# Optimization experiments

Hardware: AMD Instinct MI355X
Metric: run time of the kernel (lower is better)

The kernel has to match this reference:

```python
import jax, jax.numpy as jnp
import numpy as np

B, C, H, W = 8, 64, 128, 128
G, DGPG = 4, 1
GD = G * DGPG          # total deformable groups = 4
COUT = 64
KH = KW = 3
K = KH * KW            # 9 kernel locations
PAD = STR = DIL = 1
HO, WO = 128, 128      # same padding, stride 1
OFFSET_SCALE = 1.0
CDG = C // GD          # channels per deformable group = 16
CPG = C // G           # input channels per conv group = 16
KOFF = 7
POFF = 3


def dwconv7(x, w, b):
    # depthwise 7x7 conv, groups == channels; w: [C,1,7,7]
    y = jax.lax.conv_general_dilated(
        x, w, window_strides=(1, 1), padding=[(POFF, POFF), (POFF, POFF)],
        feature_group_count=C, dimension_numbers=('NCHW', 'OIHW', 'NCHW'))
    return y + b[None, :, None, None]


def gn1(x, g, b):
    # GroupNorm with a single group: normalize over (C,H,W) per sample
    m = x.mean(axis=(1, 2, 3), keepdims=True)
    v = x.var(axis=(1, 2, 3), keepdims=True)
    return (x - m) * jax.lax.rsqrt(v + 1e-5) * g[None, :, None, None] + b[None, :, None, None]


def pw(x, w, b):
    # 1x1 conv; w: [O, C]
    return jnp.einsum('bchw,oc->bohw', x, w) + b[None, :, None, None]


def setup_inputs() -> dict:
    key = jax.random.key(0)
    ks = jax.random.split(key, 8)
    s = 0.02
    return {
        'x': jax.random.normal(ks[0], (B, C, H, W), jnp.float32),
        'w_dw_off': jax.random.normal(ks[1], (C, 1, KOFF, KOFF), jnp.float32) * s,
        'b_dw_off': jnp.zeros((C,), jnp.float32),
        'gn_off_g': jnp.ones((C,), jnp.float32),
        'gn_off_b': jnp.zeros((C,), jnp.float32),
        'w_pw_off': jax.random.normal(ks[2], (GD * K * 2, C), jnp.float32) * s,
        'b_pw_off': jnp.zeros((GD * K * 2,), jnp.float32),
        'w_dw_m': jax.random.normal(ks[3], (C, 1, KOFF, KOFF), jnp.float32) * s,
        'b_dw_m': jnp.zeros((C,), jnp.float32),
        'gn_m_g': jnp.ones((C,), jnp.float32),
        'gn_m_b': jnp.zeros((C,), jnp.float32),
        'w_pw_m': jax.random.normal(ks[4], (GD * K, C), jnp.float32) * s,
        'b_pw_m': jnp.zeros((GD * K,), jnp.float32),
        'weight': jax.random.normal(ks[5], (COUT, CPG, KH, KW), jnp.float32) * s,
        'bias': jax.random.normal(ks[6], (COUT,), jnp.float32) * s,
    }


def _deform_conv(x, offset, mask, weight, bias):
    # offset: [B, GD, K, 2, HO, WO] (y, x); mask: [B, GD, K, HO, WO] (softmaxed)
    ky, kx = jnp.meshgrid(jnp.arange(KH), jnp.arange(KW), indexing='ij')
    ky = ky.reshape(K).astype(x.dtype)
    kx = kx.reshape(K).astype(x.dtype)
    oy = jnp.arange(HO, dtype=x.dtype)
    ox = jnp.arange(WO, dtype=x.dtype)
    base_y = oy[None, :] * STR - PAD + ky[:, None] * DIL   # [K, HO]
    base_x = ox[None, :] * STR - PAD + kx[:, None] * DIL   # [K, WO]
    py = base_y[None, None, :, :, None] + offset[:, :, :, 0] * OFFSET_SCALE  # [B,GD,K,HO,WO]
    px = base_x[None, None, :, None, :] + offset[:, :, :, 1] * OFFSET_SCALE

    x_flat = x.reshape(B, GD, CDG, H * W)
    y0 = jnp.floor(py)
    x0 = jnp.floor(px)
    wy = py - y0
    wx = px - x0

    def gather(yi, xi):
        valid = ((yi >= 0) & (yi < H) & (xi >= 0) & (xi < W)).astype(x.dtype)
        yc = jnp.clip(yi, 0, H - 1).astype(jnp.int32)
        xc = jnp.clip(xi, 0, W - 1).astype(jnp.int32)
        idx = (yc * W + xc).reshape(B, GD, 1, K * HO * WO)
        v = jnp.take_along_axis(x_flat, idx, axis=3).reshape(B, GD, CDG, K, HO, WO)
        return v * valid[:, :, None]

    v = (gather(y0, x0) * ((1 - wy) * (1 - wx))[:, :, None]
         + gather(y0, x0 + 1) * ((1 - wy) * wx)[:, :, None]
         + gather(y0 + 1, x0) * (wy * (1 - wx))[:, :, None]
         + gather(y0 + 1, x0 + 1) * (wy * wx)[:, :, None])
    v = v * mask[:, :, None]                               # modulated samples
    v = v.reshape(B, G, CPG, K, HO, WO)
    wg = weight.reshape(G, COUT // G, CPG, K)
    out = jnp.einsum('bgckhw,gock->bgohw', v, wg).reshape(B, COUT, HO, WO)
    return out + bias[None, :, None, None]


def reference(x, w_dw_off, b_dw_off, gn_off_g, gn_off_b, w_pw_off, b_pw_off,
              w_dw_m, b_dw_m, gn_m_g, gn_m_b, w_pw_m, b_pw_m, weight, bias):
    off = pw(gn1(dwconv7(x, w_dw_off, b_dw_off), gn_off_g, gn_off_b), w_pw_off, b_pw_off)
    m = pw(gn1(dwconv7(x, w_dw_m, b_dw_m), gn_m_g, gn_m_b), w_pw_m, b_pw_m)
    offset = off.reshape(B, GD, K, 2, HO, WO)
    mask = jax.nn.softmax(m.reshape(B, GD, K, HO, WO), axis=2)  # attn over kernel points
    return _deform_conv(x, offset, mask, weight, bias)
```

## Files before the change

kernel.cpp:

```cpp
#include <hip/hip_runtime.h>
#include <hip/hip_fp16.h>
#include <math.h>

#define HW     16384
#define IMG_H  128
#define IMG_W  128

typedef _Float16 f16x2 __attribute__((ext_vector_type(2)));
typedef __fp16 fp16v2 __attribute__((ext_vector_type(2)));
typedef _Float16 f16x4 __attribute__((ext_vector_type(4)));
typedef float f32x4 __attribute__((ext_vector_type(4)));

#define OFF_T2    ((size_t)0)
#define OFF_XT    ((size_t)8388608)
#define OFF_WT    ((size_t)12582912)
#define OFF_PART  ((size_t)12599040)
#define OFF_WB    ((size_t)19711744)
#define OFF_WDW2  ((size_t)19716352)
#define OFF_WBO   ((size_t)19719936)
#define OFF_WBM   ((size_t)19752704)
#define OFF_DC    ((size_t)19769088)

__global__ void k_prep(const float* __restrict__ wpw_off,
                       const float* __restrict__ wpw_m,
                       const float* __restrict__ wdef,
                       const float* __restrict__ wdwo,
                       const float* __restrict__ wdwm,
                       float* __restrict__ ws) {
    int i = blockIdx.x * 256 + threadIdx.x;
    if (i < 6912) {
        int c = i / 108, o = i % 108;
        ws[OFF_WT + i] = (o < 72) ? wpw_off[o * 64 + c] : wpw_m[(o - 72) * 64 + c];
    } else if (i < 9216) {
        int j = i - 6912;
        int lane = j & 63;
        int gt = j >> 6;
        int tap = gt % 9, g = gt / 9;
        int oc = lane & 15, qh = lane >> 4;
        union { ushort h[4]; uint2 u; } pk;
#pragma unroll
        for (int jj = 0; jj < 4; ++jj) {
            float wv = wdef[((g * 16 + oc) * 16 + (4 * qh + jj)) * 9 + tap];
            pk.h[jj] = __half_as_ushort(__float2half(wv));
        }
        ((uint2*)(ws + OFF_WB))[j] = pk.u;
    } else if (i < 12800) {
        int j = i - 9216;
        int q = j & 3;
        int r = j >> 2;
        int dy = r % 7;
        int cv = (r / 7) & 1;
        int c = r / 14;
        const float* src = cv ? wdwm : wdwo;
        int dx0 = q * 2;
        float w0 = src[c * 49 + dy * 7 + dx0];
        float w1 = (dx0 + 1 < 7) ? src[c * 49 + dy * 7 + dx0 + 1] : 0.f;
        union { __half h[2]; uint u; } pk;
        pk.h[0] = __float2half(w0);
        pk.h[1] = __float2half(w1);
        ((uint*)(ws + OFF_WDW2))[j] = pk.u;
    }
}

__global__ __launch_bounds__(256) void k_trans(const float* __restrict__ x,
                                               __half* __restrict__ xT) {
    int n = blockIdx.x * 256 + threadIdx.x;
    int p = n & (HW - 1);
    int bg = n >> 14;
    const float* src = x + (size_t)bg * 16 * HW + p;
    union { __half2 h2[8]; uint4 u[2]; } pk;
#pragma unroll
    for (int i = 0; i < 8; ++i) {
        float a = src[(size_t)(2 * i) * HW];
        float bq = src[(size_t)(2 * i + 1) * HW];
        pk.h2[i] = __halves2half2(__float2half(a), __float2half(bq));
    }
    uint4* dst = (uint4*)(xT + (size_t)n * 16);
    dst[0] = pk.u[0];
    dst[1] = pk.u[1];
}

__global__ __launch_bounds__(256) void k_dw(const float* __restrict__ x,
                                            const float* __restrict__ bdwo,
                                            const float* __restrict__ bdwm,
                                            const uint* __restrict__ wdw2,
                                            uint2* __restrict__ t2p,
                                            float* __restrict__ partial) {
    int bid = blockIdx.x;
    int b = bid >> 9;
    int c2 = (bid >> 4) & 31;
    int stripe = (bid & 15) * 8;
    int t = threadIdx.x;
    int cb = t & 31;
    int row = stripe + (t >> 5);
    int c0 = c2 * 2;

    float vo[2][4], vm[2][4];
    float s1o = 0.f, s2o = 0.f, s1m = 0.f, s2m = 0.f;
    union CV { fp16v2 v; f16x2 h; };
    union WU { uint u; f16x2 h; };

#pragma unroll
    for (int ch = 0; ch < 2; ++ch) {
        int c = c0 + ch;
        const float4* pl = (const float4*)(x + ((size_t)(b * 64 + c)) * HW);
        const uint* wp = wdw2 + c * 56;
        float acco[4] = {0.f, 0.f, 0.f, 0.f};
        float accm[4] = {0.f, 0.f, 0.f, 0.f};
#pragma unroll
        for (int dy = 0; dy < 7; ++dy) {
            int iy = row - 3 + dy;
            if (iy >= 0 && iy < IMG_H) {
                const float4* prow = pl + iy * 32;
                float4 f4 = prow[cb];
                float4 f4m = prow[cb == 0 ? 0 : cb - 1];
                float4 f4p = prow[cb == 31 ? 31 : cb + 1];
                bool le = (cb == 0), re = (cb == 31);
                float v[11];
                v[0] = le ? 0.f : f4m.y;
                v[1] = le ? 0.f : f4m.z;
                v[2] = le ? 0.f : f4m.w;
                v[3] = f4.x; v[4] = f4.y; v[5] = f4.z; v[6] = f4.w;
                v[7] = re ? 0.f : f4p.x;
                v[8] = re ? 0.f : f4p.y;
                v[9] = re ? 0.f : f4p.z;
                v[10] = re ? 0.f : f4p.w;
                f16x2 hp[10];
#pragma unroll
                for (int d = 0; d < 10; ++d) {
                    CV cv;
                    cv.v = __builtin_amdgcn_cvt_pkrtz(v[d], v[d + 1]);
                    hp[d] = cv.h;
                }
#pragma unroll
                for (int cc = 0; cc < 4; ++cc) {
                    WU w0, w1, w2, w3, u0, u1, u2, u3;
                    w0.u = wp[dy * 4 + 0]; w1.u = wp[dy * 4 + 1];
                    w2.u = wp[dy * 4 + 2]; w3.u = wp[dy * 4 + 3];
                    u0.u = wp[28 + dy * 4 + 0]; u1.u = wp[28 + dy * 4 + 1];
                    u2.u = wp[28 + dy * 4 + 2]; u3.u = wp[28 + dy * 4 + 3];
                    float ao = acco[cc], am = accm[cc];
                    ao = __builtin_amdgcn_fdot2(hp[cc],     w0.h, ao, false);
                    ao = __builtin_amdgcn_fdot2(hp[cc + 2], w1.h, ao, false);
                    ao = __builtin_amdgcn_fdot2(hp[cc + 4], w2.h, ao, false);
                    ao = __builtin_amdgcn_fdot2(hp[cc + 6], w3.h, ao, false);
                    am = __builtin_amdgcn_fdot2(hp[cc],     u0.h, am, false);
                    am = __builtin_amdgcn_fdot2(hp[cc + 2], u1.h, am, false);
                    am = __builtin_amdgcn_fdot2(hp[cc + 4], u2.h, am, false);
                    am = __builtin_amdgcn_fdot2(hp[cc + 6], u3.h, am, false);
                    acco[cc] = ao; accm[cc] = am;
                }
            }
        }
        float bo = bdwo[c], bm = bdwm[c];
#pragma unroll
        for (int cc = 0; cc < 4; ++cc) {
            float o_ = acco[cc] + bo, m_ = accm[cc] + bm;
            vo[ch][cc] = o_; vm[ch][cc] = m_;
            s1o += o_; s2o += o_ * o_; s1m += m_; s2m += m_ * m_;
        }
    }

    union { uint2 u2[4]; uint4 u4[2]; } ot;
#pragma unroll
    for (int cc = 0; cc < 4; ++cc) {
        ot.u2[cc].x = (uint)__half_as_ushort(__float2half(vo[0][cc])) |
                      ((uint)__half_as_ushort(__float2half(vo[1][cc])) << 16);
        ot.u2[cc].y = (uint)__half_as_ushort(__float2half(vm[0][cc])) |
                      ((uint)__half_as_ushort(__float2half(vm[1][cc])) << 16);
    }
    uint4* dst = (uint4*)(t2p + ((size_t)(b * 32 + c2) * HW + row * IMG_W + cb * 4));
    dst[0] = ot.u4[0];
    dst[1] = ot.u4[1];

#pragma unroll
    for (int d = 32; d; d >>= 1) {
        s1o += __shfl_down(s1o, d);
        s2o += __shfl_down(s2o, d);
        s1m += __shfl_down(s1m, d);
        s2m += __shfl_down(s2m, d);
    }
    __shared__ float red[4][4];
    if ((t & 63) == 0) {
        int w = t >> 6;
        red[w][0] = s1o; red[w][1] = s2o; red[w][2] = s1m; red[w][3] = s2m;
    }
    __syncthreads();
    if (t < 4) {
        float v = red[0][t] + red[1][t] + red[2][t] + red[3][t];
        partial[(size_t)bid * 4 + t] = v;
    }
}

__global__ __launch_bounds__(256) void k_finfold(const float* __restrict__ partial,
                      const float* __restrict__ gog, const float* __restrict__ gob,
                      const float* __restrict__ gmg, const float* __restrict__ gmb,
                      const float* __restrict__ wT,
                      const float* __restrict__ bpo,
                      const float* __restrict__ bpm,
                      uint2* __restrict__ wbo,
                      uint2* __restrict__ wbm,
                      float* __restrict__ dconst) {
    __shared__ float adsh[256];
    int b = blockIdx.x, t = threadIdx.x;
    {
        const float4* pp = (const float4*)partial + (size_t)b * 512;
        float4 s = make_float4(0.f, 0.f, 0.f, 0.f);
#pragma unroll
        for (int i = 0; i < 2; ++i) {
            float4 v = pp[t + i * 256];
            s.x += v.x; s.y += v.y; s.z += v.z; s.w += v.w;
        }
#pragma unroll
        for (int d = 32; d; d >>= 1) {
            s.x += __shfl_down(s.x, d);
            s.y += __shfl_down(s.y, d);
            s.z += __shfl_down(s.z, d);
            s.w += __shfl_down(s.w, d);
        }
        __shared__ float red[4][4];
        if ((t & 63) == 0) {
            int w = t >> 6;
            red[w][0] = s.x; red[w][1] = s.y; red[w][2] = s.z; red[w][3] = s.w;
        }
        __syncthreads();
        if (t < 64) {
            float s1o = red[0][0] + red[1][0] + red[2][0] + red[3][0];
            float s2o = red[0][1] + red[1][1] + red[2][1] + red[3][1];
            float s1m = red[0][2] + red[1][2] + red[2][2] + red[3][2];
            float s2m = red[0][3] + red[1][3] + red[2][3] + red[3][3];
            int c = t;
            const float invN = 1.f / 1048576.f;
            float m_o = s1o * invN;
            float v_o = s2o * invN - m_o * m_o;
            float i_o = rsqrtf(v_o + 1e-5f);
            float m_m = s1m * invN;
            float v_m = s2m * invN - m_m * m_m;
            float i_m = rsqrtf(v_m + 1e-5f);
            adsh[c * 4 + 0] = i_o * gog[c];
            adsh[c * 4 + 1] = gob[c] - m_o * (i_o * gog[c]);
            adsh[c * 4 + 2] = i_m * gmg[c];
            adsh[c * 4 + 3] = gmb[c] - m_m * (i_m * gmg[c]);
        }
        __syncthreads();
    }
    for (int i = t; i < 2048; i += 256) {
        int lane = i & 63;
        int f = i >> 6;
        int g = f >> 3, kk = (f >> 1) & 3, nf = f & 1;
        int n = lane & 15, q = lane >> 4;
        int out = nf * 16 + n;
        union { ushort h[4]; uint2 u; } pk;
#pragma unroll
        for (int jj = 0; jj < 4; ++jj) {
            int ch = kk * 16 + 4 * q + jj;
            float w = (out < 18) ? adsh[ch * 4 + 0] * wT[ch * 108 + g * 18 + out] : 0.f;
            pk.h[jj] = __half_as_ushort(__float2half(w));
        }
        wbo[((size_t)(b * 4) + g) * 8 * 64 + (size_t)(kk * 2 + nf) * 64 + lane] = pk.u;
    }
    for (int i = t; i < 1024; i += 256) {
        int lane = i & 63;
        int f = i >> 6;
        int g = f >> 2, kk = f & 3;
        int n = lane & 15, q = lane >> 4;
        union { ushort h[4]; uint2 u; } pk;
#pragma unroll
        for (int jj = 0; jj < 4; ++jj) {
            int ch = kk * 16 + 4 * q + jj;
            float w = (n < 9) ? adsh[ch * 4 + 2] * wT[ch * 108 + 72 + g * 9 + n] : 0.f;
            pk.h[jj] = __half_as_ushort(__float2half(w));
        }
        wbm[((size_t)(b * 4) + g) * 4 * 64 + (size_t)kk * 64 + lane] = pk.u;
    }
    if (t < 108) {
        float s = (t < 72) ? bpo[t] : bpm[t - 72];
        for (int c = 0; c < 64; ++c) {
            float d = (t < 72) ? adsh[c * 4 + 1] : adsh[c * 4 + 3];
            s = fmaf(d, wT[c * 108 + t], s);
        }
        dconst[b * 108 + t] = s;
    }
}

__global__ __launch_bounds__(256, 4) void k_gthf(const uint2* __restrict__ t2p,
                                                 const uint2* __restrict__ wbo,
                                                 const uint2* __restrict__ wbm,
                                                 const float* __restrict__ dconst,
                                                 const __half* __restrict__ xT,
                                                 const uint2* __restrict__ wb,
                                                 const float* __restrict__ bias,
                                                 float* __restrict__ out) {
    __shared__ union SMem {
        struct {
            uint4 xsA[506];
            uint4 xsB[506];
            uint  slab[5120];
        } s;
        float shout[4864];
    } sm;

    int tid = threadIdx.x;
    int bid = blockIdx.x;
    int bg = bid >> 6;
    int tile = bid & 63;
    int tr = tile >> 3, tc = tile & 7;
    int r0 = tr * 16, c0 = tc * 16;
    int g = bg & 3, b = bg >> 2;
    int wr0 = r0 - 3, wc0 = c0 - 3;

    const __half* xg = xT + (size_t)bg * HW * 16;

    int sidx[2];
    uint4 sA[2], sB[2];
#pragma unroll
    for (int it = 0; it < 2; ++it) {
        int idx = tid + it * 256;
        sidx[it] = -1;
        if (idx < 484) {
            int ly = idx / 22, lx = idx - ly * 22;
            int sr = wr0 + ly; sr = sr < 0 ? 0 : (sr > 127 ? 127 : sr);
            int sc = wc0 + lx; sc = sc < 0 ? 0 : (sc > 127 ? 127 : sc);
            const uint4* src = (const uint4*)(xg + (size_t)(sr * IMG_W + sc) * 16);
            sA[it] = src[0];
            sB[it] = src[1];
            sidx[it] = ly * 23 + lx;
        }
    }

    int row = r0 + (tid >> 4), col = c0 + (tid & 15);
    int p = row * IMG_W + col;
    int lane = tid & 63, wv = tid >> 6;
    int m_idx = lane & 15, q_idx = lane >> 4;

    union BU { uint2 u; f16x4 h; };

    const uint2* wboP = wbo + ((size_t)(b * 4) + g) * 8 * 64 + lane;
    const uint2* wbmP = wbm + ((size_t)(b * 4) + g) * 4 * 64 + lane;
    f16x4 bO[8], bM[4];
#pragma unroll
    for (int i = 0; i < 8; ++i) { BU t; t.u = wboP[i * 64]; bO[i] = t.h; }
#pragma unroll
    for (int i = 0; i < 4; ++i) { BU t; t.u = wbmP[i * 64]; bM[i] = t.h; }

    uint* aslab = sm.s.slab + wv * 1280;
    const uint2* tp = t2p + (size_t)b * 32 * HW + p;

    f32x4 accO0[4], accO1[4], accM[4];
#pragma unroll
    for (int s = 0; s < 4; ++s) {
        accO0[s] = (f32x4){0.f, 0.f, 0.f, 0.f};
        accO1[s] = (f32x4){0.f, 0.f, 0.f, 0.f};
        accM[s]  = (f32x4){0.f, 0.f, 0.f, 0.f};
    }

    uint2 cur[8], nxt[8];
#pragma unroll
    for (int j = 0; j < 8; ++j) cur[j] = tp[(size_t)j * HW];

#pragma unroll
    for (int kk = 0; kk < 4; ++kk) {
        if (kk < 3) {
#pragma unroll
            for (int j = 0; j < 8; ++j) nxt[j] = tp[(size_t)((kk + 1) * 8 + j) * HW];
        }
        uint* rowp = aslab + lane * 20;
        ((uint4*)rowp)[0] = make_uint4(cur[0].x, cur[1].x, cur[2].x, cur[3].x);
        ((uint4*)rowp)[1] = make_uint4(cur[4].x, cur[5].x, cur[6].x, cur[7].x);
        ((uint4*)(rowp + 8))[0] = make_uint4(cur[0].y, cur[1].y, cur[2].y, cur[3].y);
        ((uint4*)(rowp + 8))[1] = make_uint4(cur[4].y, cur[5].y, cur[6].y, cur[7].y);
#pragma unroll
        for (int s = 0; s < 4; ++s) {
            const uint* pr = aslab + (s * 16 + m_idx) * 20 + 2 * q_idx;
            BU ao, am;
            ao.u = *(const uint2*)pr;
            am.u = *(const uint2*)(pr + 8);
            accO0[s] = __builtin_amdgcn_mfma_f32_16x16x16f16(ao.h, bO[kk * 2 + 0], accO0[s], 0, 0, 0);
            accO1[s] = __builtin_amdgcn_mfma_f32_16x16x16f16(ao.h, bO[kk * 2 + 1], accO1[s], 0, 0, 0);
            accM[s]  = __builtin_amdgcn_mfma_f32_16x16x16f16(am.h, bM[kk], accM[s], 0, 0, 0);
        }
#pragma unroll
        for (int j = 0; j < 8; ++j) cur[j] = nxt[j];
    }

#pragma unroll
    for (int it = 0; it < 2; ++it)
        if (sidx[it] >= 0) {
            sm.s.xsA[sidx[it]] = sA[it];
            sm.s.xsB[sidx[it]] = sB[it];
        }

    const float* dc = dconst + b * 108;

#pragma unroll
    for (int s = 0; s < 4; ++s)
#pragma unroll
        for (int j = 0; j < 4; ++j) {
            int px = s * 16 + 4 * q_idx + j;
            union { __half2 h2; uint u; } pk;
            pk.h2 = __halves2half2(__float2half(accO0[s][j]),
                                   __float2half(accO1[s][j]));
            aslab[px * 20 + m_idx] = pk.u;
        }
    float facc[18];
    {
        const uint4* dr = (const uint4*)(aslab + lane * 20);
        uint4 d0 = dr[0], d1 = dr[1], d2 = dr[2], d3 = dr[3];
        uint du[16] = {d0.x, d0.y, d0.z, d0.w, d1.x, d1.y, d1.z, d1.w,
                       d2.x, d2.y, d2.z, d2.w, d3.x, d3.y, d3.z, d3.w};
        union { uint u; __half2 h2; } cv;
#pragma unroll
        for (int i = 0; i < 16; ++i) {
            cv.u = du[i];
            float2 f = __half22float2(cv.h2);
            facc[i] = f.x + dc[g * 18 + i];
            if (i < 2) facc[16 + i] = f.y + dc[g * 18 + 16 + i];
        }
    }

    float macc[9];
    {
        float* fsl = (float*)aslab;
#pragma unroll
        for (int s = 0; s < 4; ++s)
#pragma unroll
            for (int j = 0; j < 4; ++j) {
                int px = s * 16 + 4 * q_idx + j;
                fsl[px * 20 + m_idx] = accM[s][j];
            }
#pragma unroll
        for (int k = 0; k < 9; ++k) macc[k] = fsl[lane * 20 + k] + dc[72 + g * 9 + k];
        float mx = macc[0];
#pragma unroll
        for (int k = 1; k < 9; ++k) mx = fmaxf(mx, macc[k]);
        float ssum = 0.f;
#pragma unroll
        for (int k = 0; k < 9; ++k) {
            float e = __expf(macc[k] - mx);
            macc[k] = e;
            ssum += e;
        }
        float inv = 1.f / ssum;
#pragma unroll
        for (int k = 0; k < 9; ++k) macc[k] *= inv;
    }

    const uint2* wbp = wb + (size_t)(g * 9) * 64 + lane;
    f16x4 bfr[9];
#pragma unroll
    for (int k = 0; k < 9; ++k) { BU t; t.u = wbp[k * 64]; bfr[k] = t.h; }

    __syncthreads();

    uint4* shvw = (uint4*)aslab + lane * 3;
    const _Float16* shvh = (const _Float16*)aslab;

    f32x4 acc[4];
#pragma unroll
    for (int s = 0; s < 4; ++s) acc[s] = (f32x4){0.f, 0.f, 0.f, 0.f};

#pragma unroll
    for (int k = 0; k < 9; ++k) {
        float mk = macc[k];
        float py = (float)(row + k / 3 - 1) + facc[k * 2 + 0];
        float px = (float)(col + k % 3 - 1) + facc[k * 2 + 1];
        float y0f = floorf(py), x0f = floorf(px);
        float wy = py - y0f, wx = px - x0f;
        int iy0 = (int)y0f, ix0 = (int)x0f;
        int iy1 = iy0 + 1, ix1 = ix0 + 1;
        float fy0 = (iy0 >= 0 && iy0 < IMG_H) ? (1.f - wy) : 0.f;
        float fy1 = (iy1 >= 0 && iy1 < IMG_H) ? wy : 0.f;
        float fx0 = (ix0 >= 0 && ix0 < IMG_W) ? (1.f - wx) : 0.f;
        float fx1 = (ix1 >= 0 && ix1 < IMG_W) ? wx : 0.f;
        __half2 f00h = __float2half2_rn(fy0 * fx0 * mk);
        __half2 f01h = __float2half2_rn(fy0 * fx1 * mk);
        __half2 f10h = __float2half2_rn(fy1 * fx0 * mk);
        __half2 f11h = __float2half2_rn(fy1 * fx1 * mk);
        int ly0 = iy0 - wr0; ly0 = ly0 < 0 ? 0 : (ly0 > 21 ? 21 : ly0);
        int ly1 = iy1 - wr0; ly1 = ly1 < 0 ? 0 : (ly1 > 21 ? 21 : ly1);
        int lx0 = ix0 - wc0; lx0 = lx0 < 0 ? 0 : (lx0 > 21 ? 21 : lx0);
        int lx1 = ix1 - wc0; lx1 = lx1 < 0 ? 0 : (lx1 > 21 ? 21 : lx1);
        int i00 = ly0 * 23 + lx0, i01 = ly0 * 23 + lx1;
        int i10 = ly1 * 23 + lx0, i11 = ly1 * 23 + lx1;
        union Q8 { uint4 u[2]; __half2 h2[8]; };
        Q8 q00, q01, q10, q11;
        q00.u[0] = sm.s.xsA[i00]; q00.u[1] = sm.s.xsB[i00];
        q01.u[0] = sm.s.xsA[i01]; q01.u[1] = sm.s.xsB[i01];
        q10.u[0] = sm.s.xsA[i10]; q10.u[1] = sm.s.xsB[i10];
        q11.u[0] = sm.s.xsA[i11]; q11.u[1] = sm.s.xsB[i11];
        union V8 { __half2 h2[4]; uint4 u; };
        V8 pa, pb;
#pragma unroll
        for (int i = 0; i < 4; ++i) {
            __half2 vh = __hmul2(f00h, q00.h2[i]);
            vh = __hfma2(f01h, q01.h2[i], vh);
            vh = __hfma2(f10h, q10.h2[i], vh);
            vh = __hfma2(f11h, q11.h2[i], vh);
            pa.h2[i] = vh;
        }
#pragma unroll
        for (int i = 4; i < 8; ++i) {
            __half2 vh = __hmul2(f00h, q00.h2[i]);
            vh = __hfma2(f01h, q01.h2[i], vh);
            vh = __hfma2(f10h, q10.h2[i], vh);
            vh = __hfma2(f11h, q11.h2[i], vh);
            pb.h2[i - 4] = vh;
        }
        shvw[0] = pa.u;
        shvw[1] = pb.u;
#pragma unroll
        for (int s = 0; s < 4; ++s) {
            f16x4 af = *(const f16x4*)(shvh +
                        ((size_t)(s * 16 + m_idx)) * 24 + q_idx * 4);
            acc[s] = __builtin_amdgcn_mfma_f32_16x16x16f16(af, bfr[k], acc[s], 0, 0, 0);
        }
    }

    __syncthreads();

#pragma unroll
    for (int s = 0; s < 4; ++s)
#pragma unroll
        for (int j = 0; j < 4; ++j)
            sm.shout[(wv * 64 + s * 16 + 4 * q_idx + j) * 19 + m_idx] = acc[s][j];

    float* outp = out + ((size_t)b * 64 + g * 16) * HW + p;
#pragma unroll
    for (int o = 0; o < 16; ++o)
        outp[(size_t)o * HW] = sm.shout[tid * 19 + o] + bias[g * 16 + o];
}

extern "C" void kernel_launch(void* const* d_in, const int* in_sizes, int n_in,
                              void* d_out, int out_size, void* d_ws, size_t ws_size,
                              hipStream_t stream) {
    const float* x        = (const float*)d_in[0];
    const float* w_dw_off = (const float*)d_in[1];
    const float* b_dw_off = (const float*)d_in[2];
    const float* gn_off_g = (const float*)d_in[3];
    const float* gn_off_b = (const float*)d_in[4];
    const float* w_pw_off = (const float*)d_in[5];
    const float* b_pw_off = (const float*)d_in[6];
    const float* w_dw_m   = (const float*)d_in[7];
    const float* b_dw_m   = (const float*)d_in[8];
    const float* gn_m_g   = (const float*)d_in[9];
    const float* gn_m_b   = (const float*)d_in[10];
    const float* w_pw_m   = (const float*)d_in[11];
    const float* b_pw_m   = (const float*)d_in[12];
    const float* weight   = (const float*)d_in[13];
    const float* bias     = (const float*)d_in[14];

    float* ws = (float*)d_ws;
    uint2* t2p    = (uint2*)(ws + OFF_T2);
    __half* xT    = (__half*)(ws + OFF_XT);
    float* wT     = ws + OFF_WT;
    float* part   = ws + OFF_PART;
    const uint2* wb = (const uint2*)(ws + OFF_WB);
    const uint* wdw2 = (const uint*)(ws + OFF_WDW2);
    uint2* wbo    = (uint2*)(ws + OFF_WBO);
    uint2* wbm    = (uint2*)(ws + OFF_WBM);
    float* dconst = ws + OFF_DC;

    k_prep<<<50, 256, 0, stream>>>(w_pw_off, w_pw_m, weight, w_dw_off, w_dw_m, ws);
    k_trans<<<2048, 256, 0, stream>>>(x, xT);
    k_dw<<<4096, 256, 0, stream>>>(x, b_dw_off, b_dw_m, wdw2, t2p, part);
    k_finfold<<<8, 256, 0, stream>>>(part, gn_off_g, gn_off_b, gn_m_g, gn_m_b,
                                     wT, b_pw_off, b_pw_m, wbo, wbm, dconst);
    k_gthf<<<2048, 256, 0, stream>>>(t2p, wbo, wbm, dconst, xT, wb, bias, (float*)d_out);
}
```

Baseline: 103.7 us.

## Fuse x transpose into depthwise kernel and restructure gather kernel loads

```diff
diff --git a/kernel.cpp b/kernel.cpp
--- a/kernel.cpp
+++ b/kernel.cpp
@@ -62,29 +62,12 @@
     }
 }
 
-__global__ __launch_bounds__(256) void k_trans(const float* __restrict__ x,
-                                               __half* __restrict__ xT) {
-    int n = blockIdx.x * 256 + threadIdx.x;
-    int p = n & (HW - 1);
-    int bg = n >> 14;
-    const float* src = x + (size_t)bg * 16 * HW + p;
-    union { __half2 h2[8]; uint4 u[2]; } pk;
-#pragma unroll
-    for (int i = 0; i < 8; ++i) {
-        float a = src[(size_t)(2 * i) * HW];
-        float bq = src[(size_t)(2 * i + 1) * HW];
-        pk.h2[i] = __halves2half2(__float2half(a), __float2half(bq));
-    }
-    uint4* dst = (uint4*)(xT + (size_t)n * 16);
-    dst[0] = pk.u[0];
-    dst[1] = pk.u[1];
-}
-
 __global__ __launch_bounds__(256) void k_dw(const float* __restrict__ x,
                                             const float* __restrict__ bdwo,
                                             const float* __restrict__ bdwm,
                                             const uint* __restrict__ wdw2,
                                             uint2* __restrict__ t2p,
+                                            __half* __restrict__ xT,
                                             float* __restrict__ partial) {
     int bid = blockIdx.x;
     int b = bid >> 9;
@@ -96,6 +79,7 @@
     int c0 = c2 * 2;
 
     float vo[2][4], vm[2][4];
+    float4 cen[2];
     float s1o = 0.f, s2o = 0.f, s1m = 0.f, s2m = 0.f;
     union CV { fp16v2 v; f16x2 h; };
     union WU { uint u; f16x2 h; };
@@ -115,6 +99,7 @@
                 float4 f4 = prow[cb];
                 float4 f4m = prow[cb == 0 ? 0 : cb - 1];
                 float4 f4p = prow[cb == 31 ? 31 : cb + 1];
+                if (dy == 3) cen[ch] = f4;
                 bool le = (cb == 0), re = (cb == 31);
                 float v[11];
                 v[0] = le ? 0.f : f4m.y;
@@ -173,6 +158,19 @@
     dst[0] = ot.u4[0];
     dst[1] = ot.u4[1];
 
+    {
+        int bg = b * 4 + (c0 >> 4);
+        int cw = c0 & 15;
+        uint* xtw = (uint*)(xT + ((size_t)bg * HW + row * IMG_W + cb * 4) * 16 + cw);
+        float ca[4] = {cen[0].x, cen[0].y, cen[0].z, cen[0].w};
+        float cbv[4] = {cen[1].x, cen[1].y, cen[1].z, cen[1].w};
+#pragma unroll
+        for (int j = 0; j < 4; ++j) {
+            xtw[j * 8] = (uint)__half_as_ushort(__float2half(ca[j])) |
+                         ((uint)__half_as_ushort(__float2half(cbv[j])) << 16);
+        }
+    }
+
 #pragma unroll
     for (int d = 32; d; d >>= 1) {
         s1o += __shfl_down(s1o, d);
@@ -311,20 +309,16 @@
 
     const __half* xg = xT + (size_t)bg * HW * 16;
 
-    int sidx[2];
-    uint4 sA[2], sB[2];
 #pragma unroll
     for (int it = 0; it < 2; ++it) {
         int idx = tid + it * 256;
-        sidx[it] = -1;
         if (idx < 484) {
             int ly = idx / 22, lx = idx - ly * 22;
             int sr = wr0 + ly; sr = sr < 0 ? 0 : (sr > 127 ? 127 : sr);
             int sc = wc0 + lx; sc = sc < 0 ? 0 : (sc > 127 ? 127 : sc);
             const uint4* src = (const uint4*)(xg + (size_t)(sr * IMG_W + sc) * 16);
-            sA[it] = src[0];
-            sB[it] = src[1];
-            sidx[it] = ly * 23 + lx;
+            sm.s.xsA[ly * 23 + lx] = src[0];
+            sm.s.xsB[ly * 23 + lx] = src[1];
         }
     }
 
@@ -343,6 +337,11 @@
 #pragma unroll
     for (int i = 0; i < 4; ++i) { BU t; t.u = wbmP[i * 64]; bM[i] = t.h; }
 
+    const uint2* wbp = wb + (size_t)(g * 9) * 64 + lane;
+    f16x4 bfr[9];
+#pragma unroll
+    for (int k = 0; k < 9; ++k) { BU t; t.u = wbp[k * 64]; bfr[k] = t.h; }
+
     uint* aslab = sm.s.slab + wv * 1280;
     const uint2* tp = t2p + (size_t)b * 32 * HW + p;
 
@@ -354,21 +353,16 @@
         accM[s]  = (f32x4){0.f, 0.f, 0.f, 0.f};
     }
 
-    uint2 cur[8], nxt[8];
-#pragma unroll
-    for (int j = 0; j < 8; ++j) cur[j] = tp[(size_t)j * HW];
-
 #pragma unroll
     for (int kk = 0; kk < 4; ++kk) {
-        if (kk < 3) {
-#pragma unroll
-            for (int j = 0; j < 8; ++j) nxt[j] = tp[(size_t)((kk + 1) * 8 + j) * HW];
-        }
+        uint2 v[8];
+#pragma unroll
+        for (int j = 0; j < 8; ++j) v[j] = tp[(size_t)(kk * 8 + j) * HW];
         uint* rowp = aslab + lane * 20;
-        ((uint4*)rowp)[0] = make_uint4(cur[0].x, cur[1].x, cur[2].x, cur[3].x);
-        ((uint4*)rowp)[1] = make_uint4(cur[4].x, cur[5].x, cur[6].x, cur[7].x);
-        ((uint4*)(rowp + 8))[0] = make_uint4(cur[0].y, cur[1].y, cur[2].y, cur[3].y);
-        ((uint4*)(rowp + 8))[1] = make_uint4(cur[4].y, cur[5].y, cur[6].y, cur[7].y);
+        ((uint4*)rowp)[0] = make_uint4(v[0].x, v[1].x, v[2].x, v[3].x);
+        ((uint4*)rowp)[1] = make_uint4(v[4].x, v[5].x, v[6].x, v[7].x);
+        ((uint4*)(rowp + 8))[0] = make_uint4(v[0].y, v[1].y, v[2].y, v[3].y);
+        ((uint4*)(rowp + 8))[1] = make_uint4(v[4].y, v[5].y, v[6].y, v[7].y);
 #pragma unroll
         for (int s = 0; s < 4; ++s) {
             const uint* pr = aslab + (s * 16 + m_idx) * 20 + 2 * q_idx;
@@ -379,16 +373,7 @@
             accO1[s] = __builtin_amdgcn_mfma_f32_16x16x16f16(ao.h, bO[kk * 2 + 1], accO1[s], 0, 0, 0);
             accM[s]  = __builtin_amdgcn_mfma_f32_16x16x16f16(am.h, bM[kk], accM[s], 0, 0, 0);
         }
-#pragma unroll
-        for (int j = 0; j < 8; ++j) cur[j] = nxt[j];
-    }
-
-#pragma unroll
-    for (int it = 0; it < 2; ++it)
-        if (sidx[it] >= 0) {
-            sm.s.xsA[sidx[it]] = sA[it];
-            sm.s.xsB[sidx[it]] = sB[it];
-        }
+    }
 
     const float* dc = dconst + b * 108;
 
@@ -418,7 +403,6 @@
         }
     }
 
-    float macc[9];
     {
         float* fsl = (float*)aslab;
 #pragma unroll
@@ -428,6 +412,7 @@
                 int px = s * 16 + 4 * q_idx + j;
                 fsl[px * 20 + m_idx] = accM[s][j];
             }
+        float macc[9];
 #pragma unroll
         for (int k = 0; k < 9; ++k) macc[k] = fsl[lane * 20 + k] + dc[72 + g * 9 + k];
         float mx = macc[0];
@@ -443,91 +428,86 @@
         float inv = 1.f / ssum;
 #pragma unroll
         for (int k = 0; k < 9; ++k) macc[k] *= inv;
-    }
-
-    const uint2* wbp = wb + (size_t)(g * 9) * 64 + lane;
-    f16x4 bfr[9];
-#pragma unroll
-    for (int k = 0; k < 9; ++k) { BU t; t.u = wbp[k * 64]; bfr[k] = t.h; }
-
-    __syncthreads();
-
-    uint4* shvw = (uint4*)aslab + lane * 3;
-    const _Float16* shvh = (const _Float16*)aslab;
-
-    f32x4 acc[4];
-#pragma unroll
-    for (int s = 0; s < 4; ++s) acc[s] = (f32x4){0.f, 0.f, 0.f, 0.f};
-
-#pragma unroll
-    for (int k = 0; k < 9; ++k) {
-        float mk = macc[k];
-        float py = (float)(row + k / 3 - 1) + facc[k * 2 + 0];
-        float px = (float)(col + k % 3 - 1) + facc[k * 2 + 1];
-        float y0f = floorf(py), x0f = floorf(px);
-        float wy = py - y0f, wx = px - x0f;
-        int iy0 = (int)y0f, ix0 = (int)x0f;
-        int iy1 = iy0 + 1, ix1 = ix0 + 1;
-        float fy0 = (iy0 >= 0 && iy0 < IMG_H) ? (1.f - wy) : 0.f;
-        float fy1 = (iy1 >= 0 && iy1 < IMG_H) ? wy : 0.f;
-        float fx0 = (ix0 >= 0 && ix0 < IMG_W) ? (1.f - wx) : 0.f;
-        float fx1 = (ix1 >= 0 && ix1 < IMG_W) ? wx : 0.f;
-        __half2 f00h = __float2half2_rn(fy0 * fx0 * mk);
-        __half2 f01h = __float2half2_rn(fy0 * fx1 * mk);
-        __half2 f10h = __float2half2_rn(fy1 * fx0 * mk);
-        __half2 f11h = __float2half2_rn(fy1 * fx1 * mk);
-        int ly0 = iy0 - wr0; ly0 = ly0 < 0 ? 0 : (ly0 > 21 ? 21 : ly0);
-        int ly1 = iy1 - wr0; ly1 = ly1 < 0 ? 0 : (ly1 > 21 ? 21 : ly1);
-        int lx0 = ix0 - wc0; lx0 = lx0 < 0 ? 0 : (lx0 > 21 ? 21 : lx0);
-        int lx1 = ix1 - wc0; lx1 = lx1 < 0 ? 0 : (lx1 > 21 ? 21 : lx1);
-        int i00 = ly0 * 23 + lx0, i01 = ly0 * 23 + lx1;
-        int i10 = ly1 * 23 + lx0, i11 = ly1 * 23 + lx1;
-        union Q8 { uint4 u[2]; __half2 h2[8]; };
-        Q8 q00, q01, q10, q11;
-        q00.u[0] = sm.s.xsA[i00]; q00.u[1] = sm.s.xsB[i00];
-        q01.u[0] = sm.s.xsA[i01]; q01.u[1] = sm.s.xsB[i01];
-        q10.u[0] = sm.s.xsA[i10]; q10.u[1] = sm.s.xsB[i10];
-        q11.u[0] = sm.s.xsA[i11]; q11.u[1] = sm.s.xsB[i11];
-        union V8 { __half2 h2[4]; uint4 u; };
-        V8 pa, pb;
-#pragma unroll
-        for (int i = 0; i < 4; ++i) {
-            __half2 vh = __hmul2(f00h, q00.h2[i]);
-            vh = __hfma2(f01h, q01.h2[i], vh);
-            vh = __hfma2(f10h, q10.h2[i], vh);
-            vh = __hfma2(f11h, q11.h2[i], vh);
-            pa.h2[i] = vh;
-        }
-#pragma unroll
-        for (int i = 4; i < 8; ++i) {
-            __half2 vh = __hmul2(f00h, q00.h2[i]);
-            vh = __hfma2(f01h, q01.h2[i], vh);
-            vh = __hfma2(f10h, q10.h2[i], vh);
-            vh = __hfma2(f11h, q11.h2[i], vh);
-            pb.h2[i - 4] = vh;
-        }
-        shvw[0] = pa.u;
-        shvw[1] = pb.u;
-#pragma unroll
-        for (int s = 0; s < 4; ++s) {
-            f16x4 af = *(const f16x4*)(shvh +
-                        ((size_t)(s * 16 + m_idx)) * 24 + q_idx * 4);
-            acc[s] = __builtin_amdgcn_mfma_f32_16x16x16f16(af, bfr[k], acc[s], 0, 0, 0);
-        }
-    }
-
-    __syncthreads();
-
-#pragma unroll
-    for (int s = 0; s < 4; ++s)
-#pragma unroll
-        for (int j = 0; j < 4; ++j)
-            sm.shout[(wv * 64 + s * 16 + 4 * q_idx + j) * 19 + m_idx] = acc[s][j];
-
-    float* outp = out + ((size_t)b * 64 + g * 16) * HW + p;
-#pragma unroll
-    for (int o = 0; o < 16; ++o)
-        outp[(size_t)o * HW] = sm.shout[tid * 19 + o] + bias[g * 16 + o];
+
+        __syncthreads();
+
+        uint4* shvw = (uint4*)aslab + lane * 3;
+        const _Float16* shvh = (const _Float16*)aslab;
+
+        f32x4 acc[4];
+#pragma unroll
+        for (int s = 0; s < 4; ++s) acc[s] = (f32x4){0.f, 0.f, 0.f, 0.f};
+
+#pragma unroll
+        for (int k = 0; k < 9; ++k) {
+            float mk = macc[k];
+            float py = (float)(row + k / 3 - 1) + facc[k * 2 + 0];
+            float px = (float)(col + k % 3 - 1) + facc[k * 2 + 1];
+            float y0f = floorf(py), x0f = floorf(px);
+            float wy = py - y0f, wx = px - x0f;
+            int iy0 = (int)y0f, ix0 = (int)x0f;
+            int iy1 = iy0 + 1, ix1 = ix0 + 1;
+            float fy0 = (iy0 >= 0 && iy0 < IMG_H) ? (1.f - wy) : 0.f;
+            float fy1 = (iy1 >= 0 && iy1 < IMG_H) ? wy : 0.f;
+            float fx0 = (ix0 >= 0 && ix0 < IMG_W) ? (1.f - wx) : 0.f;
+            float fx1 = (ix1 >= 0 && ix1 < IMG_W) ? wx : 0.f;
+            __half2 f00h = __float2half2_rn(fy0 * fx0 * mk);
+            __half2 f01h = __float2half2_rn(fy0 * fx1 * mk);
+            __half2 f10h = __float2half2_rn(fy1 * fx0 * mk);
+            __half2 f11h = __float2half2_rn(fy1 * fx1 * mk);
+            int ly0 = iy0 - wr0; ly0 = ly0 < 0 ? 0 : (ly0 > 21 ? 21 : ly0);
+            int ly1 = iy1 - wr0; ly1 = ly1 < 0 ? 0 : (ly1 > 21 ? 21 : ly1);
+            int lx0 = ix0 - wc0; lx0 = lx0 < 0 ? 0 : (lx0 > 21 ? 21 : lx0);
+            int lx1 = ix1 - wc0; lx1 = lx1 < 0 ? 0 : (lx1 > 21 ? 21 : lx1);
+            int i00 = ly0 * 23 + lx0, i01 = ly0 * 23 + lx1;
+            int i10 = ly1 * 23 + lx0, i11 = ly1 * 23 + lx1;
+            union Q8 { uint4 u[2]; __half2 h2[8]; };
+            Q8 q00, q01, q10, q11;
+            q00.u[0] = sm.s.xsA[i00]; q00.u[1] = sm.s.xsB[i00];
+            q01.u[0] = sm.s.xsA[i01]; q01.u[1] = sm.s.xsB[i01];
+            q10.u[0] = sm.s.xsA[i10]; q10.u[1] = sm.s.xsB[i10];
+            q11.u[0] = sm.s.xsA[i11]; q11.u[1] = sm.s.xsB[i11];
+            union V8 { __half2 h2[4]; uint4 u; };
+            V8 pa, pb;
+#pragma unroll
+            for (int i = 0; i < 4; ++i) {
+                __half2 vh = __hmul2(f00h, q00.h2[i]);
+                vh = __hfma2(f01h, q01.h2[i], vh);
+                vh = __hfma2(f10h, q10.h2[i], vh);
+                vh = __hfma2(f11h, q11.h2[i], vh);
+                pa.h2[i] = vh;
+            }
+#pragma unroll
+            for (int i = 4; i < 8; ++i) {
+                __half2 vh = __hmul2(f00h, q00.h2[i]);
+                vh = __hfma2(f01h, q01.h2[i], vh);
+                vh = __hfma2(f10h, q10.h2[i], vh);
+                vh = __hfma2(f11h, q11.h2[i], vh);
+                pb.h2[i - 4] = vh;
+            }
+            shvw[0] = pa.u;
+            shvw[1] = pb.u;
+#pragma unroll
+            for (int s = 0; s < 4; ++s) {
+                f16x4 af = *(const f16x4*)(shvh +
+                            ((size_t)(s * 16 + m_idx)) * 24 + q_idx * 4);
+                acc[s] = __builtin_amdgcn_mfma_f32_16x16x16f16(af, bfr[k], acc[s], 0, 0, 0);
+            }
+        }
+
+        __syncthreads();
+
+#pragma unroll
+        for (int s = 0; s < 4; ++s)
+#pragma unroll
+            for (int j = 0; j < 4; ++j)
+                sm.shout[(wv * 64 + s * 16 + 4 * q_idx + j) * 19 + m_idx] = acc[s][j];
+
+        float* outp = out + ((size_t)b * 64 + g * 16) * HW + p;
+#pragma unroll
+        for (int o = 0; o < 16; ++o)
+            outp[(size_t)o * HW] = sm.shout[tid * 19 + o] + bias[g * 16 + o];
+    }
 }
 
 extern "C" void kernel_launch(void* const* d_in, const int* in_sizes, int n_in,
@@ -561,8 +541,7 @@
     float* dconst = ws + OFF_DC;
 
     k_prep<<<50, 256, 0, stream>>>(w_pw_off, w_pw_m, weight, w_dw_off, w_dw_m, ws);
-    k_trans<<<2048, 256, 0, stream>>>(x, xT);
-    k_dw<<<4096, 256, 0, stream>>>(x, b_dw_off, b_dw_m, wdw2, t2p, part);
+    k_dw<<<4096, 256, 0, stream>>>(x, b_dw_off, b_dw_m, wdw2, t2p, xT, part);
     k_finfold<<<8, 256, 0, stream>>>(part, gn_off_g, gn_off_b, gn_m_g, gn_m_b,
                                      wT, b_pw_off, b_pw_m, wbo, wbm, dconst);
     k_gthf<<<2048, 256, 0, stream>>>(t2p, wbo, wbm, dconst, xT, wb, bias, (float*)d_out);
```

Result: no change. 102.3 us (-1.4%).
